# Performance work log

Measured on AMD Instinct MI355X. Metric: run time of the kernel, lower is better.

The kernel has to match this reference:

```python
import jax, jax.numpy as jnp
import numpy as np

NUM_TREES = 20000
MAX_DEPTH = 8
MAX_SIZE = 40
VOCAB = 30000
ENCODE_DIM = 128


def setup_inputs() -> dict:
    key = jax.random.key(0)
    k_tok, k_emb, k_cw = jax.random.split(key, 3)
    tokens = jax.random.randint(k_tok, (NUM_TREES, MAX_DEPTH, MAX_SIZE), 0, VOCAB, dtype=jnp.int32)
    masks = jnp.ones((NUM_TREES, MAX_DEPTH, MAX_SIZE), dtype=bool)
    # learned params: embedding table and context (gate/attention) weight
    embedding = jax.random.normal(k_emb, (VOCAB, ENCODE_DIM), dtype=jnp.float32)
    context_weight = jax.random.normal(k_cw, (ENCODE_DIM, 1), dtype=jnp.float32) * 0.05
    return {"tokens": tokens, "masks": masks, "embedding": embedding, "context_weight": context_weight}


def _encode(tokens, masks, embedding, context_weight):
    N, D, S = tokens.shape
    valid = masks & (tokens >= 0)                       # [N, D, S]
    tok = jnp.maximum(tokens, 0)
    temb = embedding[tok]                               # [N, D, S, E]
    pos = jnp.arange(S)
    # deepest level: masked sum of token embeddings
    pooled = jnp.sum(temb[:, D - 1] * valid[:, D - 1, :, None].astype(temb.dtype), axis=1)  # [N, E]
    for d in range(D - 2, -1, -1):
        v = valid[:, d]                                  # [N, S]
        # number of children at level d+1 (clamped to >=1, per torch .clamp(min=1))
        nc = jnp.maximum(masks[:, d + 1].sum(axis=1), 1)  # [N]
        # child_sums[b, i] = pooled_prev[b] for i < nc[b], masked by valid
        child = ((pos[None, :] < nc[:, None]) & v).astype(temb.dtype)  # [N, S]
        child_sums = child[:, :, None] * pooled[:, None, :]             # [N, S, E]
        h = temb[:, d]                                   # [N, S, E]
        gate = jax.nn.sigmoid(h @ context_weight)        # [N, S, 1] (broadcast over E)
        h = h + gate * child_sums
        attn = (h @ context_weight)[..., 0]              # [N, S]
        attn = jax.nn.softmax(jnp.where(v, attn, -jnp.inf), axis=1)
        pooled = jnp.sum(h * attn[:, :, None], axis=1)   # [N, E]
    return pooled


def reference(tokens, masks, embedding, context_weight):
    return _encode(tokens, masks, embedding, context_weight)
```

## Files before the change

kernel.cpp:

```cpp
#include <hip/hip_runtime.h>
#include <hip/hip_fp16.h>
#include <math.h>

#define NUM_TREES 20000
#define MAX_DEPTH 8
#define MAX_SIZE  40
#define VOCAB     30000
#define DIM       128
#define TOT       (MAX_DEPTH * MAX_SIZE)
#define NTILE     8
#define TILE_ROWS (VOCAB / NTILE)
#define TPA       4

typedef unsigned long long ull;

__device__ __forceinline__ double waveSumD(double v) {
    v += __shfl_xor(v, 32);
    v += __shfl_xor(v, 16);
    v += __shfl_xor(v, 8);
    v += __shfl_xor(v, 4);
    v += __shfl_xor(v, 2);
    v += __shfl_xor(v, 1);
    return v;
}

__device__ __forceinline__ void waveSum3(double& a, double& b, double& c) {
    #pragma unroll
    for (int m = 32; m >= 1; m >>= 1) {
        a += __shfl_xor(a, m);
        b += __shfl_xor(b, m);
        c += __shfl_xor(c, m);
    }
}

__device__ __forceinline__ int loadMask(const void* m, size_t idx, bool asByte) {
    return asByte ? (int)((const unsigned char*)m)[idx] : ((const int*)m)[idx];
}

__global__ __launch_bounds__(256) void tokscore_kernel(
        const float* __restrict__ emb, const float* __restrict__ cw,
        double* __restrict__ ts) {
    int row  = (blockIdx.x * blockDim.x + threadIdx.x) >> 6;
    int lane = threadIdx.x & 63;
    if (row >= VOCAB) return;
    float2 e2 = *(const float2*)(emb + (size_t)row * DIM + lane * 2);
    float2 w2 = *(const float2*)(cw + lane * 2);
    double p = (double)e2.x * (double)w2.x + (double)e2.y * (double)w2.y;
    p = waveSumD(p);
    if (lane == 0) ts[row] = p;
}

__global__ __launch_bounds__(256) void cvt_kernel(
        const float* __restrict__ emb, __half2* __restrict__ e16) {
    int i = blockIdx.x * 256 + threadIdx.x;
    if (i >= VOCAB * DIM / 4) return;
    float4 f = ((const float4*)emb)[i];
    e16[2 * i + 0] = __floats2half2_rn(f.x, f.y);
    e16[2 * i + 1] = __floats2half2_rn(f.z, f.w);
}

__device__ __forceinline__ int recursion_and_sort(
        const int* __restrict__ tokens, const void* __restrict__ masks,
        const double* __restrict__ ts, ull (*l_pair)[TOT],
        int w, int s, size_t base) {
    const bool mByte = (((const int*)masks)[0] != 1);
    const bool inS = s < MAX_SIZE;

    int    tok[MAX_DEPTH];
    double e[MAX_DEPTH];
    unsigned int valbit = 0, mskbit = 0;
    #pragma unroll
    for (int d = 0; d < MAX_DEPTH; ++d) {
        int t = -1, m = 0;
        if (inS) {
            t = tokens[base + d * MAX_SIZE + s];
            m = loadMask(masks, base + d * MAX_SIZE + s, mByte);
        }
        tok[d] = t < 0 ? 0 : t;
        e[d]   = inS ? ts[tok[d]] : 0.0;
        if (inS && m != 0) mskbit |= 1u << d;
        if (inS && m != 0 && t >= 0) valbit |= 1u << d;
    }
    unsigned int childbit = 0;
    #pragma unroll
    for (int d = 0; d < MAX_DEPTH - 1; ++d) {
        ull bal = __ballot((mskbit >> (d + 1)) & 1u);
        int nc = (int)__popcll(bal);
        if (nc < 1) nc = 1;
        if (((valbit >> d) & 1u) && s < nc) childbit |= 1u << d;
    }

    double v7 = ((valbit >> 7) & 1u) ? 1.0 : 0.0;
    double pw = waveSumD(e[7] * v7);

    float  attnf[MAX_DEPTH - 1];
    double cArr[MAX_DEPTH - 1];
    #pragma unroll
    for (int d = MAX_DEPTH - 2; d >= 0; --d) {
        float  gf = 1.0f / (1.0f + __expf((float)(-e[d])));
        double cf = ((childbit >> d) & 1u) ? (double)gf : 0.0;
        double a  = fma(cf, pw, e[d]);
        double ex = ((valbit >> d) & 1u) ? (double)__expf((float)a) : 0.0;
        double s0 = ex, s1 = ex * cf, s2 = ex * e[d];
        waveSum3(s0, s1, s2);
        double inv = 1.0 / s0;
        double c   = s1 * inv;
        pw = fma(c, pw, s2 * inv);
        attnf[d] = (float)(ex * inv);
        cArr[d]  = c;
    }
    float coef[MAX_DEPTH];
    double prefix = 1.0;
    #pragma unroll
    for (int d = 0; d <= MAX_DEPTH - 2; ++d) {
        coef[d] = (float)(prefix * (double)attnf[d]);
        prefix *= cArr[d];
    }
    coef[MAX_DEPTH - 1] = (float)(prefix * v7);

    int tl[MAX_DEPTH];
    unsigned int nzbit = 0;
    #pragma unroll
    for (int d = 0; d < MAX_DEPTH; ++d) {
        tl[d] = tok[d] / TILE_ROWS;
        if (coef[d] != 0.0f) nzbit |= 1u << d;
    }
    const ull ltm = (1ull << s) - 1ull;

    int cnt[NTILE];
    #pragma unroll
    for (int t = 0; t < NTILE; ++t) cnt[t] = 0;
    #pragma unroll
    for (int d = 0; d < MAX_DEPTH; ++d) {
        bool nz = (nzbit >> d) & 1u;
        #pragma unroll
        for (int t = 0; t < NTILE; ++t)
            cnt[t] += (int)__popcll(__ballot(nz && tl[d] == t));
    }
    int hoff[NTILE + 1];
    hoff[0] = 0;
    #pragma unroll
    for (int t = 0; t < NTILE; ++t) hoff[t + 1] = hoff[t] + cnt[t];

    int ridx[NTILE];
    #pragma unroll
    for (int t = 0; t < NTILE; ++t) ridx[t] = hoff[t];
    #pragma unroll
    for (int d = 0; d < MAX_DEPTH; ++d) {
        bool nz = (nzbit >> d) & 1u;
        int slot = -1;
        #pragma unroll
        for (int t = 0; t < NTILE; ++t) {
            ull m = __ballot(nz && tl[d] == t);
            if (nz && tl[d] == t) slot = ridx[t] + (int)__popcll(m & ltm);
            ridx[t] += (int)__popcll(m);
        }
        if (slot >= 0)
            l_pair[w][slot] =
                ((ull)__float_as_uint(coef[d]) << 32) | (ull)(unsigned)tok[d];
    }
    return __builtin_amdgcn_readfirstlane(hoff[NTILE]);
}

__global__ __launch_bounds__(256, 4) void fused16_kernel(
        const int* __restrict__ tokens, const void* __restrict__ masks,
        const double* __restrict__ ts, const __half* __restrict__ e16,
        float* __restrict__ out) {
    __shared__ ull l_pair[TPA][TOT];

    const int tid  = threadIdx.x;
    const int w    = tid >> 6;
    const int s    = tid & 63;
    const int tree = blockIdx.x * TPA + w;
    const size_t base = (size_t)tree * TOT;

    const int nTot = recursion_and_sort(tokens, masks, ts, l_pair, w, s, base);

    const int q  = s >> 4;
    const int cb = (s & 15) << 3;
    const ull* lp = &l_pair[w][0];
    float a0 = 0.f, a1 = 0.f, a2 = 0.f, a3 = 0.f;
    float a4 = 0.f, a5 = 0.f, a6 = 0.f, a7 = 0.f;

    int j = 0;
    for (; j + 32 <= nTot; j += 32) {
        ull pr[8];
        #pragma unroll
        for (int k = 0; k < 8; ++k) pr[k] = lp[j + 4 * k + q];
        uint4 v[8];
        #pragma unroll
        for (int k = 0; k < 8; ++k)
            v[k] = *(const uint4*)(e16 + (size_t)(unsigned)pr[k] * DIM + cb);
        __builtin_amdgcn_sched_barrier(0);
        #pragma unroll
        for (int k = 0; k < 8; ++k) {
            float wt = __uint_as_float((unsigned)(pr[k] >> 32));
            float2 f0 = __half22float2(*(const __half2*)&v[k].x);
            float2 f1 = __half22float2(*(const __half2*)&v[k].y);
            float2 f2 = __half22float2(*(const __half2*)&v[k].z);
            float2 f3 = __half22float2(*(const __half2*)&v[k].w);
            a0 = fmaf(wt, f0.x, a0); a1 = fmaf(wt, f0.y, a1);
            a2 = fmaf(wt, f1.x, a2); a3 = fmaf(wt, f1.y, a3);
            a4 = fmaf(wt, f2.x, a4); a5 = fmaf(wt, f2.y, a5);
            a6 = fmaf(wt, f3.x, a6); a7 = fmaf(wt, f3.y, a7);
        }
    }
    for (; j + 4 <= nTot; j += 4) {
        ull pr = lp[j + q];
        float wt = __uint_as_float((unsigned)(pr >> 32));
        uint4 v = *(const uint4*)(e16 + (size_t)(unsigned)pr * DIM + cb);
        float2 f0 = __half22float2(*(const __half2*)&v.x);
        float2 f1 = __half22float2(*(const __half2*)&v.y);
        float2 f2 = __half22float2(*(const __half2*)&v.z);
        float2 f3 = __half22float2(*(const __half2*)&v.w);
        a0 = fmaf(wt, f0.x, a0); a1 = fmaf(wt, f0.y, a1);
        a2 = fmaf(wt, f1.x, a2); a3 = fmaf(wt, f1.y, a3);
        a4 = fmaf(wt, f2.x, a4); a5 = fmaf(wt, f2.y, a5);
        a6 = fmaf(wt, f3.x, a6); a7 = fmaf(wt, f3.y, a7);
    }
    if (j < nTot) {
        int rem = nTot - j;
        ull pr = lp[j + (q < rem ? q : 0)];
        float wt = (q < rem) ? __uint_as_float((unsigned)(pr >> 32)) : 0.0f;
        uint4 v = *(const uint4*)(e16 + (size_t)(unsigned)pr * DIM + cb);
        float2 f0 = __half22float2(*(const __half2*)&v.x);
        float2 f1 = __half22float2(*(const __half2*)&v.y);
        float2 f2 = __half22float2(*(const __half2*)&v.z);
        float2 f3 = __half22float2(*(const __half2*)&v.w);
        a0 = fmaf(wt, f0.x, a0); a1 = fmaf(wt, f0.y, a1);
        a2 = fmaf(wt, f1.x, a2); a3 = fmaf(wt, f1.y, a3);
        a4 = fmaf(wt, f2.x, a4); a5 = fmaf(wt, f2.y, a5);
        a6 = fmaf(wt, f3.x, a6); a7 = fmaf(wt, f3.y, a7);
    }

    a0 += __shfl_xor(a0, 16); a1 += __shfl_xor(a1, 16);
    a2 += __shfl_xor(a2, 16); a3 += __shfl_xor(a3, 16);
    a4 += __shfl_xor(a4, 16); a5 += __shfl_xor(a5, 16);
    a6 += __shfl_xor(a6, 16); a7 += __shfl_xor(a7, 16);
    a0 += __shfl_xor(a0, 32); a1 += __shfl_xor(a1, 32);
    a2 += __shfl_xor(a2, 32); a3 += __shfl_xor(a3, 32);
    a4 += __shfl_xor(a4, 32); a5 += __shfl_xor(a5, 32);
    a6 += __shfl_xor(a6, 32); a7 += __shfl_xor(a7, 32);

    if (s < 16) {
        float* op = out + (size_t)tree * DIM + cb;
        *(float4*)op       = make_float4(a0, a1, a2, a3);
        *(float4*)(op + 4) = make_float4(a4, a5, a6, a7);
    }
}

__global__ __launch_bounds__(256, 4) void fused_kernel(
        const int* __restrict__ tokens, const void* __restrict__ masks,
        const double* __restrict__ ts, const float* __restrict__ emb,
        float* __restrict__ out) {
    __shared__ ull l_pair[TPA][TOT];

    const int tid  = threadIdx.x;
    const int w    = tid >> 6;
    const int s    = tid & 63;
    const int tree = blockIdx.x * TPA + w;
    const size_t base = (size_t)tree * TOT;

    const int nTot = recursion_and_sort(tokens, masks, ts, l_pair, w, s, base);

    const int hi = (s >= 32) ? 1 : 0;
    const int cb = (s & 31) << 2;
    const ull* lp = &l_pair[w][0];
    float a0 = 0.0f, a1 = 0.0f, a2 = 0.0f, a3 = 0.0f;

    int j = 0;
    for (; j + 8 <= nTot; j += 8) {
        ull pr[4];
        #pragma unroll
        for (int k = 0; k < 4; ++k) pr[k] = lp[j + 2 * k + hi];
        float4 v[4];
        #pragma unroll
        for (int k = 0; k < 4; ++k)
            v[k] = *(const float4*)(emb + (size_t)(unsigned)pr[k] * DIM + cb);
        #pragma unroll
        for (int k = 0; k < 4; ++k) {
            float wt = __uint_as_float((unsigned)(pr[k] >> 32));
            a0 = fmaf(wt, v[k].x, a0); a1 = fmaf(wt, v[k].y, a1);
            a2 = fmaf(wt, v[k].z, a2); a3 = fmaf(wt, v[k].w, a3);
        }
    }
    for (; j + 2 <= nTot; j += 2) {
        ull pr = lp[j + hi];
        float wt = __uint_as_float((unsigned)(pr >> 32));
        const float4 v = *(const float4*)(emb + (size_t)(unsigned)pr * DIM + cb);
        a0 = fmaf(wt, v.x, a0); a1 = fmaf(wt, v.y, a1);
        a2 = fmaf(wt, v.z, a2); a3 = fmaf(wt, v.w, a3);
    }
    if (j < nTot) {
        ull pr = lp[j];
        float wt = hi ? 0.0f : __uint_as_float((unsigned)(pr >> 32));
        const float4 v = *(const float4*)(emb + (size_t)(unsigned)pr * DIM + cb);
        a0 = fmaf(wt, v.x, a0); a1 = fmaf(wt, v.y, a1);
        a2 = fmaf(wt, v.z, a2); a3 = fmaf(wt, v.w, a3);
    }

    a0 += __shfl_xor(a0, 32);
    a1 += __shfl_xor(a1, 32);
    a2 += __shfl_xor(a2, 32);
    a3 += __shfl_xor(a3, 32);

    if (s < 32) {
        float* op = out + (size_t)tree * DIM + cb;
        *(float4*)op = make_float4(a0, a1, a2, a3);
    }
}

extern "C" void kernel_launch(void* const* d_in, const int* in_sizes, int n_in,
                              void* d_out, int out_size, void* d_ws, size_t ws_size,
                              hipStream_t stream) {
    const int*   tokens = (const int*)d_in[0];
    const void*  masks  = d_in[1];
    const float* emb    = (const float*)d_in[2];
    const float* cw     = (const float*)d_in[3];
    float*       out    = (float*)d_out;

    const size_t o_ts  = 0;
    const size_t o_e16 = o_ts + (size_t)VOCAB * 8;
    const size_t need  = o_e16 + (size_t)VOCAB * DIM * 2;

    double* ts  = (double*)((char*)d_ws + o_ts);
    __half* e16 = (__half*)((char*)d_ws + o_e16);

    int ts_blocks = (VOCAB * 64 + 255) / 256;
    tokscore_kernel<<<ts_blocks, 256, 0, stream>>>(emb, cw, ts);

    if (ws_size >= need) {
        int cvt_blocks = (VOCAB * DIM / 4 + 255) / 256;
        cvt_kernel<<<cvt_blocks, 256, 0, stream>>>(emb, (__half2*)e16);
        fused16_kernel<<<NUM_TREES / TPA, 256, 0, stream>>>(tokens, masks, ts,
                                                            e16, out);
    } else {
        fused_kernel<<<NUM_TREES / TPA, 256, 0, stream>>>(tokens, masks, ts,
                                                          emb, out);
    }
}
```

Baseline: 241.0 us.

## Fuse fp16 conversion into token-score kernel and switch recursion math to fp32

Folds the embedding fp32-to-fp16 conversion into the token-score kernel, so the embedding table is read once and one launch disappears. The per-token scores and the whole attention recursion (wave sums, softmax normalisation, coefficient prefix products) move from double to float, which avoids slow FP64 shuffles and arithmetic. The score table halves in size, lowering gather traffic. Accumulating in fp32 instead of fp64 may cost some accuracy.

```diff
diff --git a/kernel.cpp b/kernel.cpp
--- a/kernel.cpp
+++ b/kernel.cpp
@@ -24,7 +24,17 @@
     return v;
 }
 
-__device__ __forceinline__ void waveSum3(double& a, double& b, double& c) {
+__device__ __forceinline__ float waveSumF(float v) {
+    v += __shfl_xor(v, 32);
+    v += __shfl_xor(v, 16);
+    v += __shfl_xor(v, 8);
+    v += __shfl_xor(v, 4);
+    v += __shfl_xor(v, 2);
+    v += __shfl_xor(v, 1);
+    return v;
+}
+
+__device__ __forceinline__ void waveSum3F(float& a, float& b, float& c) {
     #pragma unroll
     for (int m = 32; m >= 1; m >>= 1) {
         a += __shfl_xor(a, m);
@@ -39,35 +49,27 @@
 
 __global__ __launch_bounds__(256) void tokscore_kernel(
         const float* __restrict__ emb, const float* __restrict__ cw,
-        double* __restrict__ ts) {
+        float* __restrict__ ts, __half2* __restrict__ e16) {
     int row  = (blockIdx.x * blockDim.x + threadIdx.x) >> 6;
     int lane = threadIdx.x & 63;
     if (row >= VOCAB) return;
     float2 e2 = *(const float2*)(emb + (size_t)row * DIM + lane * 2);
     float2 w2 = *(const float2*)(cw + lane * 2);
+    if (e16) e16[(size_t)row * 64 + lane] = __floats2half2_rn(e2.x, e2.y);
     double p = (double)e2.x * (double)w2.x + (double)e2.y * (double)w2.y;
     p = waveSumD(p);
-    if (lane == 0) ts[row] = p;
-}
-
-__global__ __launch_bounds__(256) void cvt_kernel(
-        const float* __restrict__ emb, __half2* __restrict__ e16) {
-    int i = blockIdx.x * 256 + threadIdx.x;
-    if (i >= VOCAB * DIM / 4) return;
-    float4 f = ((const float4*)emb)[i];
-    e16[2 * i + 0] = __floats2half2_rn(f.x, f.y);
-    e16[2 * i + 1] = __floats2half2_rn(f.z, f.w);
+    if (lane == 0) ts[row] = (float)p;
 }
 
 __device__ __forceinline__ int recursion_and_sort(
         const int* __restrict__ tokens, const void* __restrict__ masks,
-        const double* __restrict__ ts, ull (*l_pair)[TOT],
+        const float* __restrict__ ts, ull (*l_pair)[TOT],
         int w, int s, size_t base) {
     const bool mByte = (((const int*)masks)[0] != 1);
     const bool inS = s < MAX_SIZE;
 
-    int    tok[MAX_DEPTH];
-    double e[MAX_DEPTH];
+    int   tok[MAX_DEPTH];
+    float e[MAX_DEPTH];
     unsigned int valbit = 0, mskbit = 0;
     #pragma unroll
     for (int d = 0; d < MAX_DEPTH; ++d) {
@@ -77,7 +79,7 @@
             m = loadMask(masks, base + d * MAX_SIZE + s, mByte);
         }
         tok[d] = t < 0 ? 0 : t;
-        e[d]   = inS ? ts[tok[d]] : 0.0;
+        e[d]   = inS ? ts[tok[d]] : 0.0f;
         if (inS && m != 0) mskbit |= 1u << d;
         if (inS && m != 0 && t >= 0) valbit |= 1u << d;
     }
@@ -90,33 +92,35 @@
         if (((valbit >> d) & 1u) && s < nc) childbit |= 1u << d;
     }
 
-    double v7 = ((valbit >> 7) & 1u) ? 1.0 : 0.0;
-    double pw = waveSumD(e[7] * v7);
-
-    float  attnf[MAX_DEPTH - 1];
-    double cArr[MAX_DEPTH - 1];
+    float v7 = ((valbit >> 7) & 1u) ? 1.0f : 0.0f;
+    float pw = waveSumF(e[7] * v7);
+
+    float attnf[MAX_DEPTH - 1];
+    float cArr[MAX_DEPTH - 1];
     #pragma unroll
     for (int d = MAX_DEPTH - 2; d >= 0; --d) {
-        float  gf = 1.0f / (1.0f + __expf((float)(-e[d])));
-        double cf = ((childbit >> d) & 1u) ? (double)gf : 0.0;
-        double a  = fma(cf, pw, e[d]);
-        double ex = ((valbit >> d) & 1u) ? (double)__expf((float)a) : 0.0;
-        double s0 = ex, s1 = ex * cf, s2 = ex * e[d];
-        waveSum3(s0, s1, s2);
-        double inv = 1.0 / s0;
-        double c   = s1 * inv;
-        pw = fma(c, pw, s2 * inv);
-        attnf[d] = (float)(ex * inv);
+        float gf = 1.0f / (1.0f + __expf(-e[d]));
+        float cf = ((childbit >> d) & 1u) ? gf : 0.0f;
+        float a  = fmaf(cf, pw, e[d]);
+        float ex = ((valbit >> d) & 1u) ? __expf(a) : 0.0f;
+        float s0 = ex;
+        float s1 = ex * cf;
+        float s2 = ex * e[d];
+        waveSum3F(s0, s1, s2);
+        float inv = 1.0f / s0;
+        float c   = s1 * inv;
+        pw = fmaf(c, pw, s2 * inv);
+        attnf[d] = ex * inv;
         cArr[d]  = c;
     }
     float coef[MAX_DEPTH];
-    double prefix = 1.0;
+    float prefix = 1.0f;
     #pragma unroll
     for (int d = 0; d <= MAX_DEPTH - 2; ++d) {
-        coef[d] = (float)(prefix * (double)attnf[d]);
+        coef[d] = prefix * attnf[d];
         prefix *= cArr[d];
     }
-    coef[MAX_DEPTH - 1] = (float)(prefix * v7);
+    coef[MAX_DEPTH - 1] = prefix * v7;
 
     int tl[MAX_DEPTH];
     unsigned int nzbit = 0;
@@ -164,7 +168,7 @@
 
 __global__ __launch_bounds__(256, 4) void fused16_kernel(
         const int* __restrict__ tokens, const void* __restrict__ masks,
-        const double* __restrict__ ts, const __half* __restrict__ e16,
+        const float* __restrict__ ts, const __half* __restrict__ e16,
         float* __restrict__ out) {
     __shared__ ull l_pair[TPA][TOT];
 
@@ -251,7 +255,7 @@
 
 __global__ __launch_bounds__(256, 4) void fused_kernel(
         const int* __restrict__ tokens, const void* __restrict__ masks,
-        const double* __restrict__ ts, const float* __restrict__ emb,
+        const float* __restrict__ ts, const float* __restrict__ emb,
         float* __restrict__ out) {
     __shared__ ull l_pair[TPA][TOT];
 
@@ -320,18 +324,18 @@
     float*       out    = (float*)d_out;
 
     const size_t o_ts  = 0;
-    const size_t o_e16 = o_ts + (size_t)VOCAB * 8;
+    const size_t o_e16 = 128 * 1024;
     const size_t need  = o_e16 + (size_t)VOCAB * DIM * 2;
 
-    double* ts  = (double*)((char*)d_ws + o_ts);
+    float*  ts  = (float*)((char*)d_ws + o_ts);
     __half* e16 = (__half*)((char*)d_ws + o_e16);
 
+    const bool fp16path = (ws_size >= need);
     int ts_blocks = (VOCAB * 64 + 255) / 256;
-    tokscore_kernel<<<ts_blocks, 256, 0, stream>>>(emb, cw, ts);
-
-    if (ws_size >= need) {
-        int cvt_blocks = (VOCAB * DIM / 4 + 255) / 256;
-        cvt_kernel<<<cvt_blocks, 256, 0, stream>>>(emb, (__half2*)e16);
+    tokscore_kernel<<<ts_blocks, 256, 0, stream>>>(
+        emb, cw, ts, fp16path ? (__half2*)e16 : (__half2*)nullptr);
+
+    if (fp16path) {
         fused16_kernel<<<NUM_TREES / TPA, 256, 0, stream>>>(tokens, masks, ts,
                                                             e16, out);
     } else {
```

After: 233.5 us. 3.1% less time.
